# Kernel tuning notes

Measured on AMD Instinct MI355X. Metric: run time of the kernel, lower is better.

## Reference

```python
import jax, jax.numpy as jnp
import numpy as np

B, T, I = 64, 512, 512      # batch, timesteps, input feature dim
H1, H2 = 256, 128           # prenet hiddens
C = 1024                    # GRU channels
M = 80                      # mel bins
L = 2                       # residual GRU layers


def setup_inputs() -> dict:
    key = jax.random.key(0)
    ks = jax.random.split(key, 10)
    s = 0.02
    w = lambda k, shape: (jax.random.normal(k, shape, jnp.float32) * s)
    return {
        "inputs": jax.random.normal(ks[0], (B, T, I), jnp.float32),
        # prenet: Linear(M->H1) + ReLU, Linear(H1->H2) + ReLU (dropout off / eval)
        "pre_w0": w(ks[1], (H1, M)), "pre_b0": jnp.zeros((H1,), jnp.float32),
        "pre_w1": w(ks[2], (H2, H1)), "pre_b1": jnp.zeros((H2,), jnp.float32),
        # attention GRU: input I+H2 -> C (PyTorch gate layout [r|z|n])
        "attn_w_ih": w(ks[3], (3 * C, I + H2)), "attn_w_hh": w(ks[4], (3 * C, C)),
        "attn_b_ih": jnp.zeros((3 * C,), jnp.float32), "attn_b_hh": jnp.zeros((3 * C,), jnp.float32),
        # L residual GRUs: C -> C, stacked on leading axis
        "gru_w_ih": w(ks[5], (L, 3 * C, C)), "gru_w_hh": w(ks[6], (L, 3 * C, C)),
        "gru_b_ih": jnp.zeros((L, 3 * C), jnp.float32), "gru_b_hh": jnp.zeros((L, 3 * C), jnp.float32),
        # projection C -> M
        "proj_w": w(ks[7], (M, C)), "proj_b": jnp.zeros((M,), jnp.float32),
    }


def gru_cell(x, h, w_ih, w_hh, b_ih, b_hh):
    # PyTorch GRUCell math, gates ordered [r, z, n]
    gi = x @ w_ih.T + b_ih
    gh = h @ w_hh.T + b_hh
    i_r, i_z, i_n = jnp.split(gi, 3, axis=-1)
    h_r, h_z, h_n = jnp.split(gh, 3, axis=-1)
    r = jax.nn.sigmoid(i_r + h_r)
    z = jax.nn.sigmoid(i_z + h_z)
    n = jnp.tanh(i_n + r * h_n)
    return (1.0 - z) * n + z * h


def reference(inputs, pre_w0, pre_b0, pre_w1, pre_b1,
              attn_w_ih, attn_w_hh, attn_b_ih, attn_b_hh,
              gru_w_ih, gru_w_hh, gru_b_ih, gru_b_hh,
              proj_w, proj_b):
    bsz = inputs.shape[0]
    chan = attn_w_hh.shape[1]
    nlayers = gru_w_ih.shape[0]
    mel = proj_w.shape[0]

    def step(carry, feat):  # feat: [B, I]
        frame, attnh, hidd = carry  # [B,M], [B,C], [L,B,C]
        # prenet on previous frame (dropout disabled, eval-mode reference)
        p = jax.nn.relu(jax.nn.relu(frame @ pre_w0.T + pre_b0) @ pre_w1.T + pre_b1)
        attnh = gru_cell(jnp.concatenate([feat, p], axis=-1), attnh,
                         attn_w_ih, attn_w_hh, attn_b_ih, attn_b_hh)
        x = attnh
        new_hidd = []
        for l in range(nlayers):  # small fixed layer count
            h = gru_cell(x, hidd[l], gru_w_ih[l], gru_w_hh[l], gru_b_ih[l], gru_b_hh[l])
            x = x + h
            new_hidd.append(h)
        frame = x @ proj_w.T + proj_b
        return (frame, attnh, jnp.stack(new_hidd)), frame

    init = (jnp.zeros((bsz, mel), inputs.dtype),
            jnp.zeros((bsz, chan), inputs.dtype),
            jnp.zeros((nlayers, bsz, chan), inputs.dtype))
    _, frames = jax.lax.scan(step, init, jnp.swapaxes(inputs, 0, 1))  # [T,B,M]
    return jnp.swapaxes(frames, 0, 1)  # [B,T,M]
```

## Files before the change

### kernel.cpp

```cpp
#include <hip/hip_runtime.h>
#include <cstddef>


namespace {

constexpr int kB = 64, kT = 512, kI = 512, kH1 = 256, kH2 = 128, kC = 1024, kM = 80;

typedef __attribute__((ext_vector_type(8))) __bf16 bf16x8;
typedef __attribute__((ext_vector_type(4))) float f32x4;

__device__ __forceinline__ float sigm(float x) { return 1.0f / (1.0f + __expf(-x)); }
__device__ __forceinline__ float tanh_(float x) {
  float a = fabsf(x);
  float e = __expf(-2.0f * a);
  float r = (1.0f - e) / (1.0f + e);
  return copysignf(r, x);
}
__device__ __forceinline__ unsigned short f2bf(float x) {
  unsigned u = __builtin_bit_cast(unsigned, x);
  u += 0x7fffu + ((u >> 16) & 1u);
  return (unsigned short)(u >> 16);
}
__device__ __forceinline__ bf16x8 asbf(uint4 v) { return __builtin_bit_cast(bf16x8, v); }
__device__ __forceinline__ f32x4 mfma16(bf16x8 a, bf16x8 b, f32x4 c) {
  return __builtin_amdgcn_mfma_f32_16x16x32_bf16(a, b, c, 0, 0, 0);
}

__global__ __launch_bounds__(256) void k_build_frags(
    const float* __restrict__ srcA, int ldA,
    const float* __restrict__ srcB, int ldB,
    int row0, int K1, int nks, int nrt, unsigned short* __restrict__ dst) {
  int idx = blockIdx.x * 256 + threadIdx.x;
  int lane = idx & 63;
  int ks = (idx >> 6) % nks;
  int rt = idx / (64 * nks);
  if (rt >= nrt) return;
  int row = row0 + rt * 16 + (lane & 15);
  int kk = ks * 32 + ((lane >> 4) & 3) * 8;
  const float* s = (kk < K1) ? (srcA + (size_t)row * ldA + kk)
                             : (srcB + (size_t)row * ldB + (kk - K1));
  unsigned short* d = dst + ((size_t)(rt * nks + ks) * 64 + lane) * 8;
#pragma unroll
  for (int j = 0; j < 8; ++j) d[j] = f2bf(s[j]);
}

__global__ __launch_bounds__(256) void k_transpose(const float* __restrict__ src,
    int R, int Ccols, float* __restrict__ dst) {
  int i = blockIdx.x * 256 + threadIdx.x;
  if (i >= R * Ccols) return;
  int r = i / Ccols, c = i % Ccols;
  dst[c * R + r] = src[r * Ccols + c];
}

__global__ __launch_bounds__(256) void k_prenet(
    const float* __restrict__ inputs, int t,
    const float* __restrict__ pproj,
    const float* __restrict__ proj_b,
    const float* __restrict__ w0t, const float* __restrict__ b0,
    const float* __restrict__ w1t, const float* __restrict__ b1,
    unsigned short* __restrict__ xcat0_cur,
    float* __restrict__ out_frames) {
  int b = blockIdx.x, tid = threadIdx.x;
  __shared__ float sfr[kM];
  __shared__ float sh[kH1];
  __shared__ float sred[160];
  const float* feat = inputs + ((size_t)b * kT + t) * kI;
  unsigned short* dst = xcat0_cur + (size_t)b * 1664;
  float2 f2v = *(const float2*)(feat + tid * 2);
  dst[tid * 2] = f2bf(f2v.x);
  dst[tid * 2 + 1] = f2bf(f2v.y);
  if (t > 0) {
    if (tid < 160) {
      int m = tid >> 1, half = tid & 1;
      const float* pp = pproj + ((size_t)(half * 32) * kM + m) * kB + b;
      float s = 0.0f;
#pragma unroll 8
      for (int r = 0; r < 32; ++r) s += pp[(size_t)r * kM * kB];
      sred[tid] = s;
    }
    __syncthreads();
    if (tid < kM) {
      float f = proj_b[tid] + sred[tid * 2] + sred[tid * 2 + 1];
      sfr[tid] = f;
      out_frames[(size_t)b * kT * kM + (size_t)(t - 1) * kM + tid] = f;
    }
  } else {
    if (tid < kM) sfr[tid] = 0.0f;
  }
  __syncthreads();
  float acc = b0[tid];
#pragma unroll 8
  for (int m = 0; m < kM; ++m) acc = fmaf(w0t[m * kH1 + tid], sfr[m], acc);
  sh[tid] = fmaxf(acc, 0.0f);
  __syncthreads();
  if (tid < kH2) {
    float a = b1[tid];
#pragma unroll 8
    for (int k = 0; k < kH1; ++k) a = fmaf(w1t[k * kH2 + tid], sh[k], a);
    dst[512 + tid] = f2bf(fmaxf(a, 0.0f));
  }
}

template<int NKS, int NB, int BROW>
__global__ __launch_bounds__(512) void k_gru(
    const unsigned short* __restrict__ Ar, const unsigned short* __restrict__ Az,
    const unsigned short* __restrict__ An,
    const unsigned short* __restrict__ Bsrc,
    const float* __restrict__ h_old,
    const float* __restrict__ bih, const float* __restrict__ bhh,
    const float* __restrict__ xin_f32,
    float* __restrict__ h_new_f32,
    unsigned short* __restrict__ h_bf16, int hStride, int hOff,
    unsigned short* __restrict__ x_bf16, int xStride,
    float* __restrict__ xout_f32,
    const float* __restrict__ pw, float* __restrict__ pproj) {
  __shared__ float red[8 * 4 * 64 * 4];
  __shared__ float sx[16 * 16];
  int tid = threadIdx.x;
  int lane = tid & 63, w = tid >> 6, quad = lane >> 4;
  int xcd = blockIdx.x & 7, slot = blockIdx.x >> 3;
  int rt = xcd * 8 + (slot >> 2);
  int bt = slot & 3;
  int b = bt * 16 + (lane & 15);
  int s = (w * NKS) >> 3, e = ((w + 1) * NKS) >> 3;
  const uint4* Bq = (const uint4*)Bsrc + (size_t)b * BROW + quad;
  const uint4* Arq = (const uint4*)Ar + (size_t)rt * NKS * 64 + lane;
  const uint4* Azq = (const uint4*)Az + (size_t)rt * NKS * 64 + lane;
  const uint4* Anq = (const uint4*)An + (size_t)rt * NKS * 64 + lane;
  f32x4 aR = {0.f, 0.f, 0.f, 0.f}, aZ = aR, aNI = aR, aNH = aR;
  for (int ks = s; ks < e; ++ks) {
    bf16x8 bv = asbf(Bq[ks * 4]);
    aR = mfma16(asbf(Arq[ks * 64]), bv, aR);
    aZ = mfma16(asbf(Azq[ks * 64]), bv, aZ);
    if (ks < NB) aNI = mfma16(asbf(Anq[ks * 64]), bv, aNI);
    else         aNH = mfma16(asbf(Anq[ks * 64]), bv, aNH);
  }
  *(f32x4*)(red + ((w * 4 + 0) * 64 + lane) * 4) = aR;
  *(f32x4*)(red + ((w * 4 + 1) * 64 + lane) * 4) = aZ;
  *(f32x4*)(red + ((w * 4 + 2) * 64 + lane) * 4) = aNI;
  *(f32x4*)(red + ((w * 4 + 3) * 64 + lane) * 4) = aNH;
  __syncthreads();
  if (w < 4) {
    int q = lane >> 4, bb = lane & 15;
    float R = 0.f, Z = 0.f, NI = 0.f, NH = 0.f;
#pragma unroll
    for (int ww = 0; ww < 8; ++ww) {
      int base = (ww * 4 * 64 + w * 16 + bb) * 4 + q;
      R  += red[base];
      Z  += red[base + 64 * 4];
      NI += red[base + 2 * 64 * 4];
      NH += red[base + 3 * 64 * 4];
    }
    int c = rt * 16 + w * 4 + q;
    float r = sigm(R + bih[c] + bhh[c]);
    float z = sigm(Z + bih[kC + c] + bhh[kC + c]);
    float n = tanh_(NI + bih[2 * kC + c] + r * (NH + bhh[2 * kC + c]));
    float hold = h_old[c * kB + b];
    float hn = (1.0f - z) * n + z * hold;
    h_new_f32[c * kB + b] = hn;
    h_bf16[(size_t)b * hStride + hOff + c] = f2bf(hn);
    float xo = xin_f32 ? (xin_f32[c * kB + b] + hn) : hn;
    if (x_bf16) x_bf16[(size_t)b * xStride + c] = f2bf(xo);
    if (xout_f32) xout_f32[c * kB + b] = xo;
    if (pw) sx[(w * 4 + q) * 16 + bb] = xo;
  }
  if (pw) {
    __syncthreads();
    for (int idx = tid; idx < kM * 16; idx += 512) {
      int m = idx >> 4, bb = idx & 15;
      const float* wrow = pw + (size_t)m * kC + rt * 16;
      float a = 0.f;
#pragma unroll
      for (int c16 = 0; c16 < 16; ++c16) a += wrow[c16] * sx[c16 * 16 + bb];
      pproj[((size_t)rt * kM + m) * kB + bt * 16 + bb] = a;
    }
  }
}

__global__ __launch_bounds__(256) void k_finalize(const float* __restrict__ pproj,
    const float* __restrict__ proj_b, float* __restrict__ out) {
  int idx = blockIdx.x * 256 + threadIdx.x;
  if (idx >= kB * kM) return;
  int b = idx / kM, m = idx % kM;
  float s = proj_b[m];
#pragma unroll 8
  for (int rt = 0; rt < 64; ++rt) s += pproj[((size_t)rt * kM + m) * kB + b];
  out[(size_t)b * kT * kM + (size_t)(kT - 1) * kM + m] = s;
}

}

extern "C" void kernel_launch(void* const* d_in, const int* in_sizes, int n_in,
                              void* d_out, int out_size, void* d_ws, size_t ws_size,
                              hipStream_t stream) {
  const float* inputs   = (const float*)d_in[0];
  const float* pre_w0   = (const float*)d_in[1];
  const float* pre_b0   = (const float*)d_in[2];
  const float* pre_w1   = (const float*)d_in[3];
  const float* pre_b1   = (const float*)d_in[4];
  const float* attn_wih = (const float*)d_in[5];
  const float* attn_whh = (const float*)d_in[6];
  const float* attn_bih = (const float*)d_in[7];
  const float* attn_bhh = (const float*)d_in[8];
  const float* gru_wih  = (const float*)d_in[9];
  const float* gru_whh  = (const float*)d_in[10];
  const float* gru_bih  = (const float*)d_in[11];
  const float* gru_bhh  = (const float*)d_in[12];
  const float* proj_w   = (const float*)d_in[13];
  const float* proj_b   = (const float*)d_in[14];
  float* out = (float*)d_out;
  char* ws = (char*)d_ws;

  const size_t ATTN_MAT = (size_t)64 * 52 * 64 * 8 * 2;
  const size_t RES_MAT  = (size_t)64 * 64 * 64 * 8 * 2;
  size_t off = 0;
  unsigned short* Aattn[3];
  for (int g = 0; g < 3; ++g) { Aattn[g] = (unsigned short*)(ws + off); off += ATTN_MAT; }
  unsigned short* Ares[2][3];
  for (int l = 0; l < 2; ++l)
    for (int g = 0; g < 3; ++g) { Ares[l][g] = (unsigned short*)(ws + off); off += RES_MAT; }
  float* w0t = (float*)(ws + off); off += (size_t)kM * kH1 * 4;
  float* w1t = (float*)(ws + off); off += (size_t)kH1 * kH2 * 4;
  float* pproj = (float*)(ws + off); off += (size_t)64 * kM * kB * 4;
  size_t zeroBase = off;
  unsigned short* xcat0 = (unsigned short*)(ws + off); off += 2 * (size_t)kB * 1664 * 2;
  unsigned short* xcat1 = (unsigned short*)(ws + off); off += 2 * (size_t)kB * 2048 * 2;
  unsigned short* xcat2 = (unsigned short*)(ws + off); off += 2 * (size_t)kB * 2048 * 2;
  const size_t HB = (size_t)kC * kB;
  float* hA = (float*)(ws + off); off += 2 * HB * 4;
  float* h1 = (float*)(ws + off); off += 2 * HB * 4;
  float* h2 = (float*)(ws + off); off += 2 * HB * 4;
  float* x1 = (float*)(ws + off); off += HB * 4;
  if (off > ws_size) return;

  for (int g = 0; g < 3; ++g)
    k_build_frags<<<16 * 52, 256, 0, stream>>>(attn_wih, 640, attn_whh, kC,
                                               g * kC, 640, 52, 64, Aattn[g]);
  for (int l = 0; l < 2; ++l) {
    const float* wih = gru_wih + (size_t)l * 3 * kC * kC;
    const float* whh = gru_whh + (size_t)l * 3 * kC * kC;
    for (int g = 0; g < 3; ++g)
      k_build_frags<<<16 * 64, 256, 0, stream>>>(wih, kC, whh, kC,
                                                 g * kC, kC, 64, 64, Ares[l][g]);
  }
  k_transpose<<<(kH1 * kM + 255) / 256, 256, 0, stream>>>(pre_w0, kH1, kM, w0t);
  k_transpose<<<(kH2 * kH1 + 255) / 256, 256, 0, stream>>>(pre_w1, kH2, kH1, w1t);
  hipMemsetAsync(ws + zeroBase, 0, off - zeroBase, stream);

  const size_t X0 = (size_t)kB * 1664;
  const size_t XC = (size_t)kB * 2048;
  const float* g_bih1 = gru_bih + 3 * kC;
  const float* g_bhh1 = gru_bhh + 3 * kC;

  for (int t = 0; t < kT; ++t) {
    int cur = t & 1, nxt = cur ^ 1;
    k_prenet<<<kB, 256, 0, stream>>>(inputs, t, pproj, proj_b,
                                     w0t, pre_b0, w1t, pre_b1,
                                     xcat0 + cur * X0, out);
    k_gru<52, 20, 208><<<256, 512, 0, stream>>>(Aattn[0], Aattn[1], Aattn[2],
        xcat0 + cur * X0, hA + cur * HB, attn_bih, attn_bhh,
        nullptr, hA + nxt * HB,
        xcat0 + nxt * X0, 1664, 640,
        xcat1 + cur * XC, 2048,
        nullptr, nullptr, nullptr);
    k_gru<64, 32, 256><<<256, 512, 0, stream>>>(Ares[0][0], Ares[0][1], Ares[0][2],
        xcat1 + cur * XC, h1 + cur * HB, gru_bih, gru_bhh,
        hA + nxt * HB, h1 + nxt * HB,
        xcat1 + nxt * XC, 2048, 1024,
        xcat2 + cur * XC, 2048,
        x1, nullptr, nullptr);
    k_gru<64, 32, 256><<<256, 512, 0, stream>>>(Ares[1][0], Ares[1][1], Ares[1][2],
        xcat2 + cur * XC, h2 + cur * HB, g_bih1, g_bhh1,
        x1, h2 + nxt * HB,
        xcat2 + nxt * XC, 2048, 1024,
        nullptr, 0,
        nullptr, proj_w, pproj);
  }
  k_finalize<<<(kB * kM + 255) / 256, 256, 0, stream>>>(pproj, proj_b, out);
}
```

Baseline: 22.13 ms.

## Fuse per-timestep kernels into one persistent cooperative kernel with grid barriers

Replaces the per-timestep launches of the prenet and three GRU kernels with one cooperative persistent kernel. It loops over all timesteps and separates phases with an atomic-counter grid barrier. The goal is to remove launch and inter-kernel gap overhead across roughly two thousand launches. In exchange it relies on all 256 blocks being co-resident and adds the cost of spin-wait barrier synchronisation.

```diff
diff --git a/kernel.cpp b/kernel.cpp
--- a/kernel.cpp
+++ b/kernel.cpp
@@ -5,6 +5,9 @@
 namespace {
 
 constexpr int kB = 64, kT = 512, kI = 512, kH1 = 256, kH2 = 128, kC = 1024, kM = 80;
+constexpr size_t X0 = (size_t)kB * 1664;
+constexpr size_t XC = (size_t)kB * 2048;
+constexpr size_t HB = (size_t)kC * kB;
 
 typedef __attribute__((ext_vector_type(8))) __bf16 bf16x8;
 typedef __attribute__((ext_vector_type(4))) float f32x4;
@@ -52,27 +55,49 @@
   dst[c * R + r] = src[r * Ccols + c];
 }
 
-__global__ __launch_bounds__(256) void k_prenet(
-    const float* __restrict__ inputs, int t,
-    const float* __restrict__ pproj,
-    const float* __restrict__ proj_b,
-    const float* __restrict__ w0t, const float* __restrict__ b0,
-    const float* __restrict__ w1t, const float* __restrict__ b1,
-    unsigned short* __restrict__ xcat0_cur,
-    float* __restrict__ out_frames) {
+struct KParams {
+  const float* inputs;
+  const float* proj_b;
+  const float* w0t;
+  const float* pre_b0;
+  const float* w1t;
+  const float* pre_b1;
+  const unsigned short* Aat0; const unsigned short* Aat1; const unsigned short* Aat2;
+  const unsigned short* Ar00; const unsigned short* Ar01; const unsigned short* Ar02;
+  const unsigned short* Ar10; const unsigned short* Ar11; const unsigned short* Ar12;
+  const float* attn_bih; const float* attn_bhh;
+  const float* g_bih0; const float* g_bhh0;
+  const float* g_bih1; const float* g_bhh1;
+  const float* proj_w;
+  unsigned short* xcat0; unsigned short* xcat1; unsigned short* xcat2;
+  float* hA; float* h1; float* h2; float* x1; float* pproj; float* out;
+  unsigned* bar;
+};
+
+__device__ __forceinline__ void gsync(unsigned* bar, unsigned target) {
+  __syncthreads();
+  if (threadIdx.x == 0) {
+    __threadfence();
+    __hip_atomic_fetch_add(bar, 1u, __ATOMIC_RELAXED, __HIP_MEMORY_SCOPE_AGENT);
+    while (__hip_atomic_load(bar, __ATOMIC_RELAXED, __HIP_MEMORY_SCOPE_AGENT) < target)
+      __builtin_amdgcn_s_sleep(2);
+    __threadfence();
+  }
+  __syncthreads();
+}
+
+__device__ __forceinline__ void prenet_phase(const KParams& p, int t, float* smem) {
+  float* sfr  = smem;
+  float* sh   = smem + 96;
+  float* sred = smem + 384;
   int b = blockIdx.x, tid = threadIdx.x;
-  __shared__ float sfr[kM];
-  __shared__ float sh[kH1];
-  __shared__ float sred[160];
-  const float* feat = inputs + ((size_t)b * kT + t) * kI;
-  unsigned short* dst = xcat0_cur + (size_t)b * 1664;
-  float2 f2v = *(const float2*)(feat + tid * 2);
-  dst[tid * 2] = f2bf(f2v.x);
-  dst[tid * 2 + 1] = f2bf(f2v.y);
+  const float* feat = p.inputs + ((size_t)b * kT + t) * kI;
+  unsigned short* dst = p.xcat0 + (size_t)(t & 1) * X0 + (size_t)b * 1664;
+  dst[tid] = f2bf(feat[tid]);
   if (t > 0) {
     if (tid < 160) {
       int m = tid >> 1, half = tid & 1;
-      const float* pp = pproj + ((size_t)(half * 32) * kM + m) * kB + b;
+      const float* pp = p.pproj + ((size_t)(half * 32) * kM + m) * kB + b;
       float s = 0.0f;
 #pragma unroll 8
       for (int r = 0; r < 32; ++r) s += pp[(size_t)r * kM * kB];
@@ -80,29 +105,32 @@
     }
     __syncthreads();
     if (tid < kM) {
-      float f = proj_b[tid] + sred[tid * 2] + sred[tid * 2 + 1];
+      float f = p.proj_b[tid] + sred[tid * 2] + sred[tid * 2 + 1];
       sfr[tid] = f;
-      out_frames[(size_t)b * kT * kM + (size_t)(t - 1) * kM + tid] = f;
+      p.out[(size_t)b * kT * kM + (size_t)(t - 1) * kM + tid] = f;
     }
   } else {
     if (tid < kM) sfr[tid] = 0.0f;
   }
   __syncthreads();
-  float acc = b0[tid];
+  if (tid < kH1) {
+    float acc = p.pre_b0[tid];
 #pragma unroll 8
-  for (int m = 0; m < kM; ++m) acc = fmaf(w0t[m * kH1 + tid], sfr[m], acc);
-  sh[tid] = fmaxf(acc, 0.0f);
+    for (int m = 0; m < kM; ++m) acc = fmaf(p.w0t[m * kH1 + tid], sfr[m], acc);
+    sh[tid] = fmaxf(acc, 0.0f);
+  }
   __syncthreads();
   if (tid < kH2) {
-    float a = b1[tid];
+    float a = p.pre_b1[tid];
 #pragma unroll 8
-    for (int k = 0; k < kH1; ++k) a = fmaf(w1t[k * kH2 + tid], sh[k], a);
+    for (int k = 0; k < kH1; ++k) a = fmaf(p.w1t[k * kH2 + tid], sh[k], a);
     dst[512 + tid] = f2bf(fmaxf(a, 0.0f));
   }
 }
 
 template<int NKS, int NB, int BROW>
-__global__ __launch_bounds__(512) void k_gru(
+__device__ __forceinline__ void gru_phase(
+    float* red, float* sx,
     const unsigned short* __restrict__ Ar, const unsigned short* __restrict__ Az,
     const unsigned short* __restrict__ An,
     const unsigned short* __restrict__ Bsrc,
@@ -114,8 +142,6 @@
     unsigned short* __restrict__ x_bf16, int xStride,
     float* __restrict__ xout_f32,
     const float* __restrict__ pw, float* __restrict__ pproj) {
-  __shared__ float red[8 * 4 * 64 * 4];
-  __shared__ float sx[16 * 16];
   int tid = threadIdx.x;
   int lane = tid & 63, w = tid >> 6, quad = lane >> 4;
   int xcd = blockIdx.x & 7, slot = blockIdx.x >> 3;
@@ -177,15 +203,47 @@
   }
 }
 
-__global__ __launch_bounds__(256) void k_finalize(const float* __restrict__ pproj,
-    const float* __restrict__ proj_b, float* __restrict__ out) {
-  int idx = blockIdx.x * 256 + threadIdx.x;
-  if (idx >= kB * kM) return;
-  int b = idx / kM, m = idx % kM;
-  float s = proj_b[m];
+__global__ __launch_bounds__(512) void k_persist(KParams p) {
+  __shared__ float red[8 * 4 * 64 * 4];
+  __shared__ float sx[16 * 16];
+  unsigned ep = 0;
+  for (int t = 0; t < kT; ++t) {
+    int cur = t & 1, nxt = cur ^ 1;
+    if (blockIdx.x < kB) prenet_phase(p, t, red);
+    gsync(p.bar, ++ep * 256);
+    gru_phase<52, 20, 208>(red, sx, p.Aat0, p.Aat1, p.Aat2,
+        p.xcat0 + (size_t)cur * X0, p.hA + (size_t)cur * HB,
+        p.attn_bih, p.attn_bhh,
+        nullptr, p.hA + (size_t)nxt * HB,
+        p.xcat0 + (size_t)nxt * X0, 1664, 640,
+        p.xcat1 + (size_t)cur * XC, 2048,
+        nullptr, nullptr, nullptr);
+    gsync(p.bar, ++ep * 256);
+    gru_phase<64, 32, 256>(red, sx, p.Ar00, p.Ar01, p.Ar02,
+        p.xcat1 + (size_t)cur * XC, p.h1 + (size_t)cur * HB,
+        p.g_bih0, p.g_bhh0,
+        p.hA + (size_t)nxt * HB, p.h1 + (size_t)nxt * HB,
+        p.xcat1 + (size_t)nxt * XC, 2048, 1024,
+        p.xcat2 + (size_t)cur * XC, 2048,
+        p.x1, nullptr, nullptr);
+    gsync(p.bar, ++ep * 256);
+    gru_phase<64, 32, 256>(red, sx, p.Ar10, p.Ar11, p.Ar12,
+        p.xcat2 + (size_t)cur * XC, p.h2 + (size_t)cur * HB,
+        p.g_bih1, p.g_bhh1,
+        p.x1, p.h2 + (size_t)nxt * HB,
+        p.xcat2 + (size_t)nxt * XC, 2048, 1024,
+        nullptr, 0,
+        nullptr, p.proj_w, p.pproj);
+    gsync(p.bar, ++ep * 256);
+  }
+  int idx = blockIdx.x * 512 + threadIdx.x;
+  if (idx < kB * kM) {
+    int b = idx / kM, m = idx % kM;
+    float s = p.proj_b[m];
 #pragma unroll 8
-  for (int rt = 0; rt < 64; ++rt) s += pproj[((size_t)rt * kM + m) * kB + b];
-  out[(size_t)b * kT * kM + (size_t)(kT - 1) * kM + m] = s;
+    for (int rt = 0; rt < 64; ++rt) s += p.pproj[((size_t)rt * kM + m) * kB + b];
+    p.out[(size_t)b * kT * kM + (size_t)(kT - 1) * kM + m] = s;
+  }
 }
 
 }
@@ -223,10 +281,10 @@
   float* w1t = (float*)(ws + off); off += (size_t)kH1 * kH2 * 4;
   float* pproj = (float*)(ws + off); off += (size_t)64 * kM * kB * 4;
   size_t zeroBase = off;
+  unsigned* bar = (unsigned*)(ws + off); off += 256;
   unsigned short* xcat0 = (unsigned short*)(ws + off); off += 2 * (size_t)kB * 1664 * 2;
   unsigned short* xcat1 = (unsigned short*)(ws + off); off += 2 * (size_t)kB * 2048 * 2;
   unsigned short* xcat2 = (unsigned short*)(ws + off); off += 2 * (size_t)kB * 2048 * 2;
-  const size_t HB = (size_t)kC * kB;
   float* hA = (float*)(ws + off); off += 2 * HB * 4;
   float* h1 = (float*)(ws + off); off += 2 * HB * 4;
   float* h2 = (float*)(ws + off); off += 2 * HB * 4;
@@ -247,34 +305,20 @@
   k_transpose<<<(kH2 * kH1 + 255) / 256, 256, 0, stream>>>(pre_w1, kH2, kH1, w1t);
   hipMemsetAsync(ws + zeroBase, 0, off - zeroBase, stream);
 
-  const size_t X0 = (size_t)kB * 1664;
-  const size_t XC = (size_t)kB * 2048;
-  const float* g_bih1 = gru_bih + 3 * kC;
-  const float* g_bhh1 = gru_bhh + 3 * kC;
-
-  for (int t = 0; t < kT; ++t) {
-    int cur = t & 1, nxt = cur ^ 1;
-    k_prenet<<<kB, 256, 0, stream>>>(inputs, t, pproj, proj_b,
-                                     w0t, pre_b0, w1t, pre_b1,
-                                     xcat0 + cur * X0, out);
-    k_gru<52, 20, 208><<<256, 512, 0, stream>>>(Aattn[0], Aattn[1], Aattn[2],
-        xcat0 + cur * X0, hA + cur * HB, attn_bih, attn_bhh,
-        nullptr, hA + nxt * HB,
-        xcat0 + nxt * X0, 1664, 640,
-        xcat1 + cur * XC, 2048,
-        nullptr, nullptr, nullptr);
-    k_gru<64, 32, 256><<<256, 512, 0, stream>>>(Ares[0][0], Ares[0][1], Ares[0][2],
-        xcat1 + cur * XC, h1 + cur * HB, gru_bih, gru_bhh,
-        hA + nxt * HB, h1 + nxt * HB,
-        xcat1 + nxt * XC, 2048, 1024,
-        xcat2 + cur * XC, 2048,
-        x1, nullptr, nullptr);
-    k_gru<64, 32, 256><<<256, 512, 0, stream>>>(Ares[1][0], Ares[1][1], Ares[1][2],
-        xcat2 + cur * XC, h2 + cur * HB, g_bih1, g_bhh1,
-        x1, h2 + nxt * HB,
-        xcat2 + nxt * XC, 2048, 1024,
-        nullptr, 0,
-        nullptr, proj_w, pproj);
-  }
-  k_finalize<<<(kB * kM + 255) / 256, 256, 0, stream>>>(pproj, proj_b, out);
-}
+  KParams kp;
+  kp.inputs = inputs; kp.proj_b = proj_b;
+  kp.w0t = w0t; kp.pre_b0 = pre_b0; kp.w1t = w1t; kp.pre_b1 = pre_b1;
+  kp.Aat0 = Aattn[0]; kp.Aat1 = Aattn[1]; kp.Aat2 = Aattn[2];
+  kp.Ar00 = Ares[0][0]; kp.Ar01 = Ares[0][1]; kp.Ar02 = Ares[0][2];
+  kp.Ar10 = Ares[1][0]; kp.Ar11 = Ares[1][1]; kp.Ar12 = Ares[1][2];
+  kp.attn_bih = attn_bih; kp.attn_bhh = attn_bhh;
+  kp.g_bih0 = gru_bih; kp.g_bhh0 = gru_bhh;
+  kp.g_bih1 = gru_bih + 3 * kC; kp.g_bhh1 = gru_bhh + 3 * kC;
+  kp.proj_w = proj_w;
+  kp.xcat0 = xcat0; kp.xcat1 = xcat1; kp.xcat2 = xcat2;
+  kp.hA = hA; kp.h1 = h1; kp.h2 = h2; kp.x1 = x1; kp.pproj = pproj; kp.out = out;
+  kp.bar = bar;
+  void* kargs[] = { (void*)&kp };
+  (void)hipLaunchCooperativeKernel(reinterpret_cast<void*>(k_persist),
+                                   dim3(256), dim3(512), kargs, 0, stream);
+}
```

After: 60.32 ms. 173% more time.
